# Kernel optimization log

Hardware: AMD Instinct MI355X
Metric: run time of the kernel (lower is better)

The kernel has to match this reference:

```python
import jax, jax.numpy as jnp
import numpy as np

FEATURE_DIM = 64
VALUE_DIM = 64
BATCH_HEADS = 64
SEQ_LEN = 4096


def setup_inputs() -> dict:
    key = jax.random.key(0)
    kq, kk, kv = jax.random.split(key, 3)
    q = jax.random.normal(kq, (BATCH_HEADS, SEQ_LEN, FEATURE_DIM), dtype=jnp.float32)
    k = jax.random.normal(kk, (BATCH_HEADS, SEQ_LEN, FEATURE_DIM), dtype=jnp.float32)
    v = jax.random.normal(kv, (BATCH_HEADS, SEQ_LEN, VALUE_DIM), dtype=jnp.float32)
    return {"q": q, "k": k, "v": v}


def reference(q, k, v):
    # q,k: (BH, S, F); v: (BH, S, V)
    # Recurrence: w_t = w_{t-1} + k_t v_t^T ; out_t = (q_t . w_t) / (t+1)
    bh, seq_len, f = q.shape
    val = v.shape[-1]

    def step(w, qkv_t):
        q_t, k_t, v_t = qkv_t  # (BH,F), (BH,F), (BH,V)
        w = w + jnp.einsum('bf,bv->bfv', k_t, v_t)
        out_t = jnp.einsum('bf,bfv->bv', q_t, w)
        return w, out_t

    w0 = jnp.zeros((bh, f, val), dtype=q.dtype)
    # scan over the sequence axis (time-major)
    xs = (jnp.swapaxes(q, 0, 1), jnp.swapaxes(k, 0, 1), jnp.swapaxes(v, 0, 1))
    _, outs = jax.lax.scan(step, w0, xs)  # outs: (S, BH, V)
    denom = jnp.arange(1, seq_len + 1, dtype=q.dtype)[:, None, None]
    outs = outs / denom
    return jnp.swapaxes(outs, 0, 1)  # (BH, S, V)
```

## Files before the change

kernel.cpp:

```cpp
#include <hip/hip_runtime.h>


#define BH    64
#define SEQ   4096
#define FD    64
#define VD    64
#define CHUNK 64
#define NCH   (SEQ / CHUNK)

typedef __attribute__((ext_vector_type(8))) short  short8;
typedef __attribute__((ext_vector_type(4))) float  f32x4;

static __device__ __forceinline__ unsigned short f2bf(float f) {
    unsigned int u = __builtin_bit_cast(unsigned int, f);
    u += 0x7FFF + ((u >> 16) & 1);
    return (unsigned short)(u >> 16);
}
static __device__ __forceinline__ float bf2f(unsigned short h) {
    unsigned int u = ((unsigned int)h) << 16;
    return __builtin_bit_cast(float, u);
}

__global__ __launch_bounds__(256) void ttr_pass1(const float* __restrict__ k,
                                                 const float* __restrict__ v,
                                                 unsigned short* __restrict__ ST) {
    const int b  = blockIdx.x >> 6;
    const int ci = blockIdx.x & 63;
    __shared__ unsigned short KT[64][72];
    __shared__ unsigned short VT[64][72];
    const int tid = threadIdx.x;
    const float* kc = k + ((size_t)b * SEQ + (size_t)ci * CHUNK) * FD;
    const float* vc = v + ((size_t)b * SEQ + (size_t)ci * CHUNK) * FD;

    #pragma unroll
    for (int i = tid; i < 64 * 16; i += 256) {
        const int s = i >> 4, f4 = (i & 15) << 2;
        float4 kv = *(const float4*)(kc + s * FD + f4);
        float4 vv = *(const float4*)(vc + s * FD + f4);
        KT[f4 + 0][s] = f2bf(kv.x); KT[f4 + 1][s] = f2bf(kv.y);
        KT[f4 + 2][s] = f2bf(kv.z); KT[f4 + 3][s] = f2bf(kv.w);
        VT[f4 + 0][s] = f2bf(vv.x); VT[f4 + 1][s] = f2bf(vv.y);
        VT[f4 + 2][s] = f2bf(vv.z); VT[f4 + 3][s] = f2bf(vv.w);
    }
    __syncthreads();

    const int wid  = tid >> 6;
    const int lane = tid & 63;
    const int mrow = lane & 15;
    const int kb   = (lane >> 4) << 3;

    f32x4 acc[4] = {};
    #pragma unroll
    for (int ks = 0; ks < 2; ks++) {
        short8 a = *(const short8*)&VT[16 * wid + mrow][ks * 32 + kb];
        #pragma unroll
        for (int cf = 0; cf < 4; cf++) {
            short8 bb = *(const short8*)&KT[16 * cf + mrow][ks * 32 + kb];
            acc[cf] = __builtin_amdgcn_mfma_f32_16x16x32_bf16(a, bb, acc[cf], 0, 0, 0);
        }
    }
    unsigned short* outp = ST + (size_t)(b * NCH + ci) * (VD * FD);
    const int vrow0 = 16 * wid + ((lane >> 4) << 2);
    const int fcol  = lane & 15;
    #pragma unroll
    for (int cf = 0; cf < 4; cf++)
        #pragma unroll
        for (int r = 0; r < 4; r++)
            outp[(size_t)(vrow0 + r) * FD + cf * 16 + fcol] = f2bf(acc[cf][r]);
}

__global__ __launch_bounds__(256) void ttr_pass2(unsigned short* __restrict__ ST) {
    const int b = blockIdx.x >> 4;
    const int e = ((blockIdx.x & 15) << 8) + threadIdx.x;
    unsigned short* p = ST + (size_t)b * NCH * (VD * FD) + e;
    float acc = 0.f;
    #pragma unroll 8
    for (int ci = 0; ci < NCH; ci++) {
        unsigned short s = p[(size_t)ci * (VD * FD)];
        p[(size_t)ci * (VD * FD)] = f2bf(acc);
        acc += bf2f(s);
    }
}

__global__ __launch_bounds__(256) void ttr_pass3(const float* __restrict__ q,
                                                 const float* __restrict__ k,
                                                 const float* __restrict__ v,
                                                 const unsigned short* __restrict__ WT,
                                                 float* __restrict__ out) {
    const int b  = blockIdx.x >> 6;
    const int ci = blockIdx.x & 63;
    __shared__ unsigned short Qs[64][72];
    __shared__ unsigned short Ks[64][72];
    __shared__ unsigned short VTs[64][136];
    __shared__ unsigned short Ps[4][16][72];
    const int tid = threadIdx.x;
    const float* qc = q + ((size_t)b * SEQ + (size_t)ci * CHUNK) * FD;
    const float* kc = k + ((size_t)b * SEQ + (size_t)ci * CHUNK) * FD;
    const float* vc = v + ((size_t)b * SEQ + (size_t)ci * CHUNK) * FD;

    #pragma unroll
    for (int i = tid; i < 64 * 16; i += 256) {
        const int t = i >> 4, f4 = (i & 15) << 2;
        float4 qv = *(const float4*)(qc + t * FD + f4);
        float4 kv = *(const float4*)(kc + t * FD + f4);
        float4 vv = *(const float4*)(vc + t * FD + f4);
        Qs[t][f4 + 0] = f2bf(qv.x); Qs[t][f4 + 1] = f2bf(qv.y);
        Qs[t][f4 + 2] = f2bf(qv.z); Qs[t][f4 + 3] = f2bf(qv.w);
        Ks[t][f4 + 0] = f2bf(kv.x); Ks[t][f4 + 1] = f2bf(kv.y);
        Ks[t][f4 + 2] = f2bf(kv.z); Ks[t][f4 + 3] = f2bf(kv.w);
        VTs[f4 + 0][t] = f2bf(vv.x); VTs[f4 + 1][t] = f2bf(vv.y);
        VTs[f4 + 2][t] = f2bf(vv.z); VTs[f4 + 3][t] = f2bf(vv.w);
    }
    const unsigned short* wsrc = WT + (size_t)(b * NCH + ci) * (VD * FD);
    #pragma unroll
    for (int i = tid; i < 512; i += 256) {
        const int vv = i >> 3, f8 = (i & 7) << 3;
        *(uint4*)&VTs[vv][64 + f8] = *(const uint4*)(wsrc + vv * FD + f8);
    }
    __syncthreads();

    const int wid  = tid >> 6;
    const int lane = tid & 63;
    const int mrow = lane & 15;
    const int kb   = (lane >> 4) << 3;

    f32x4 pacc[4] = {};
    #pragma unroll
    for (int ks = 0; ks < 2; ks++) {
        short8 a = *(const short8*)&Qs[16 * wid + mrow][ks * 32 + kb];
        #pragma unroll
        for (int cf = 0; cf < 4; cf++) {
            short8 bb = *(const short8*)&Ks[16 * cf + mrow][ks * 32 + kb];
            pacc[cf] = __builtin_amdgcn_mfma_f32_16x16x32_bf16(a, bb, pacc[cf], 0, 0, 0);
        }
    }
    const int prow0 = (lane >> 4) << 2;
    const int pcol  = lane & 15;
    #pragma unroll
    for (int cf = 0; cf < 4; cf++)
        #pragma unroll
        for (int r = 0; r < 4; r++) {
            const int row_local = 16 * wid + prow0 + r;
            const int col       = cf * 16 + pcol;
            const float val = (col <= row_local) ? pacc[cf][r] : 0.f;
            Ps[wid][prow0 + r][cf * 16 + pcol] = f2bf(val);
        }
    __syncthreads();

    f32x4 oacc[4] = {};
    #pragma unroll
    for (int ks = 0; ks < 4; ks++) {
        short8 a;
        if (ks < 2) a = *(const short8*)&Ps[wid][mrow][ks * 32 + kb];
        else        a = *(const short8*)&Qs[16 * wid + mrow][(ks - 2) * 32 + kb];
        #pragma unroll
        for (int cn = 0; cn < 4; cn++) {
            short8 bb = *(const short8*)&VTs[16 * cn + mrow][ks * 32 + kb];
            oacc[cn] = __builtin_amdgcn_mfma_f32_16x16x32_bf16(a, bb, oacc[cn], 0, 0, 0);
        }
    }
    float* oc = out + ((size_t)b * SEQ + (size_t)ci * CHUNK) * VD;
    #pragma unroll
    for (int cn = 0; cn < 4; cn++)
        #pragma unroll
        for (int r = 0; r < 4; r++) {
            const int row_local = 16 * wid + prow0 + r;
            const float den = (float)(ci * CHUNK + row_local + 1);
            oc[(size_t)row_local * VD + cn * 16 + pcol] = oacc[cn][r] / den;
        }
}

extern "C" void kernel_launch(void* const* d_in, const int* in_sizes, int n_in,
                              void* d_out, int out_size, void* d_ws, size_t ws_size,
                              hipStream_t stream) {
    const float* q = (const float*)d_in[0];
    const float* k = (const float*)d_in[1];
    const float* v = (const float*)d_in[2];
    float* out = (float*)d_out;
    unsigned short* ST = (unsigned short*)d_ws;

    ttr_pass1<<<BH * NCH, 256, 0, stream>>>(k, v, ST);
    ttr_pass2<<<BH * (SEQ / CHUNK / 4), 256, 0, stream>>>(ST);
    ttr_pass3<<<BH * NCH, 256, 0, stream>>>(q, k, v, ST, out);
}
```

Measured before the change: 258.4 us.

## Merge prefix-scan into main pass, double chunk size to 128

Removes the separate prefix-sum kernel: each main-pass block now sums all earlier chunk states itself before running the intra-chunk attention. The chunk size goes from 64 to 128, so there are half as many states and the intra-chunk causal matmul doubles. Blocks grow to 512 threads, use packed bf16 conversion, stage chunk sums through shared memory for coalesced stores, and remap block indices so heads interleave. The price is redundant state-summing work, which grows with chunk index and is quadratic in the number of chunks, plus higher shared memory use per block.

```diff
diff --git a/kernel.cpp b/kernel.cpp
--- a/kernel.cpp
+++ b/kernel.cpp
@@ -1,12 +1,12 @@
 #include <hip/hip_runtime.h>
 
 
-#define BH    64
-#define SEQ   4096
-#define FD    64
-#define VD    64
-#define CHUNK 64
-#define NCH   (SEQ / CHUNK)
+#define BH   64
+#define SEQ  4096
+#define FD   64
+#define VD   64
+#define C    128
+#define NCH  (SEQ / C)
 
 typedef __attribute__((ext_vector_type(8))) short  short8;
 typedef __attribute__((ext_vector_type(4))) float  f32x4;
@@ -20,27 +20,39 @@
     unsigned int u = ((unsigned int)h) << 16;
     return __builtin_bit_cast(float, u);
 }
-
-__global__ __launch_bounds__(256) void ttr_pass1(const float* __restrict__ k,
-                                                 const float* __restrict__ v,
-                                                 unsigned short* __restrict__ ST) {
-    const int b  = blockIdx.x >> 6;
-    const int ci = blockIdx.x & 63;
-    __shared__ unsigned short KT[64][72];
-    __shared__ unsigned short VT[64][72];
+static __device__ __forceinline__ unsigned int pk2(float lo, float hi) {
+    unsigned int a = __builtin_bit_cast(unsigned int, lo);
+    unsigned int b = __builtin_bit_cast(unsigned int, hi);
+    a += 0x7FFF + ((a >> 16) & 1);
+    b += 0x7FFF + ((b >> 16) & 1);
+    return (a >> 16) | (b & 0xFFFF0000u);
+}
+
+__global__ __launch_bounds__(512, 4) void ttr_sums(const float* __restrict__ k,
+                                                   const float* __restrict__ v,
+                                                   unsigned short* __restrict__ ST) {
+    const int b  = blockIdx.x >> 5;
+    const int ci = blockIdx.x & 31;
+    __shared__ unsigned short KT[64][136];
+    __shared__ unsigned short VT[64][136];
+    __shared__ unsigned short Cs[64][72];
     const int tid = threadIdx.x;
-    const float* kc = k + ((size_t)b * SEQ + (size_t)ci * CHUNK) * FD;
-    const float* vc = v + ((size_t)b * SEQ + (size_t)ci * CHUNK) * FD;
-
-    #pragma unroll
-    for (int i = tid; i < 64 * 16; i += 256) {
-        const int s = i >> 4, f4 = (i & 15) << 2;
-        float4 kv = *(const float4*)(kc + s * FD + f4);
-        float4 vv = *(const float4*)(vc + s * FD + f4);
-        KT[f4 + 0][s] = f2bf(kv.x); KT[f4 + 1][s] = f2bf(kv.y);
-        KT[f4 + 2][s] = f2bf(kv.z); KT[f4 + 3][s] = f2bf(kv.w);
-        VT[f4 + 0][s] = f2bf(vv.x); VT[f4 + 1][s] = f2bf(vv.y);
-        VT[f4 + 2][s] = f2bf(vv.z); VT[f4 + 3][s] = f2bf(vv.w);
+    const float* kc = k + ((size_t)b * SEQ + (size_t)ci * C) * FD;
+    const float* vc = v + ((size_t)b * SEQ + (size_t)ci * C) * FD;
+
+    #pragma unroll
+    for (int it = 0; it < 4; ++it) {
+        const int i = tid + it * 512;
+        const int f = i & 63, t4 = (i >> 6) << 2;
+        float k0 = kc[(t4+0)*FD + f], k1 = kc[(t4+1)*FD + f];
+        float k2 = kc[(t4+2)*FD + f], k3 = kc[(t4+3)*FD + f];
+        float v0 = vc[(t4+0)*FD + f], v1 = vc[(t4+1)*FD + f];
+        float v2 = vc[(t4+2)*FD + f], v3 = vc[(t4+3)*FD + f];
+        uint2 kw, vw;
+        kw.x = pk2(k0, k1); kw.y = pk2(k2, k3);
+        vw.x = pk2(v0, v1); vw.y = pk2(v2, v3);
+        *(uint2*)&KT[f][t4] = kw;
+        *(uint2*)&VT[f][t4] = vw;
     }
     __syncthreads();
 
@@ -49,73 +61,90 @@
     const int mrow = lane & 15;
     const int kb   = (lane >> 4) << 3;
 
-    f32x4 acc[4] = {};
-    #pragma unroll
-    for (int ks = 0; ks < 2; ks++) {
-        short8 a = *(const short8*)&VT[16 * wid + mrow][ks * 32 + kb];
-        #pragma unroll
-        for (int cf = 0; cf < 4; cf++) {
-            short8 bb = *(const short8*)&KT[16 * cf + mrow][ks * 32 + kb];
-            acc[cf] = __builtin_amdgcn_mfma_f32_16x16x32_bf16(a, bb, acc[cf], 0, 0, 0);
-        }
-    }
+    if (wid < 4) {
+        f32x4 acc[4] = {};
+        #pragma unroll
+        for (int ks = 0; ks < 4; ++ks) {
+            short8 a = *(const short8*)&VT[16 * wid + mrow][ks * 32 + kb];
+            #pragma unroll
+            for (int cf = 0; cf < 4; ++cf) {
+                short8 bb = *(const short8*)&KT[16 * cf + mrow][ks * 32 + kb];
+                acc[cf] = __builtin_amdgcn_mfma_f32_16x16x32_bf16(a, bb, acc[cf], 0, 0, 0);
+            }
+        }
+        const int vrow0 = 16 * wid + ((lane >> 4) << 2);
+        const int fcol  = lane & 15;
+        #pragma unroll
+        for (int cf = 0; cf < 4; ++cf)
+            #pragma unroll
+            for (int r = 0; r < 4; ++r)
+                Cs[vrow0 + r][cf * 16 + fcol] = f2bf(acc[cf][r]);
+    }
+    __syncthreads();
+
     unsigned short* outp = ST + (size_t)(b * NCH + ci) * (VD * FD);
-    const int vrow0 = 16 * wid + ((lane >> 4) << 2);
-    const int fcol  = lane & 15;
-    #pragma unroll
-    for (int cf = 0; cf < 4; cf++)
-        #pragma unroll
-        for (int r = 0; r < 4; r++)
-            outp[(size_t)(vrow0 + r) * FD + cf * 16 + fcol] = f2bf(acc[cf][r]);
-}
-
-__global__ __launch_bounds__(256) void ttr_pass2(unsigned short* __restrict__ ST) {
-    const int b = blockIdx.x >> 4;
-    const int e = ((blockIdx.x & 15) << 8) + threadIdx.x;
-    unsigned short* p = ST + (size_t)b * NCH * (VD * FD) + e;
-    float acc = 0.f;
-    #pragma unroll 8
-    for (int ci = 0; ci < NCH; ci++) {
-        unsigned short s = p[(size_t)ci * (VD * FD)];
-        p[(size_t)ci * (VD * FD)] = f2bf(acc);
-        acc += bf2f(s);
-    }
-}
-
-__global__ __launch_bounds__(256) void ttr_pass3(const float* __restrict__ q,
-                                                 const float* __restrict__ k,
-                                                 const float* __restrict__ v,
-                                                 const unsigned short* __restrict__ WT,
-                                                 float* __restrict__ out) {
-    const int b  = blockIdx.x >> 6;
-    const int ci = blockIdx.x & 63;
-    __shared__ unsigned short Qs[64][72];
-    __shared__ unsigned short Ks[64][72];
-    __shared__ unsigned short VTs[64][136];
-    __shared__ unsigned short Ps[4][16][72];
+    const int rr = tid >> 3, c8 = (tid & 7) << 3;
+    *(uint4*)(outp + rr * FD + c8) = *(const uint4*)&Cs[rr][c8];
+}
+
+__global__ __launch_bounds__(512, 4) void ttr_main(const float* __restrict__ q,
+                                                   const float* __restrict__ k,
+                                                   const float* __restrict__ v,
+                                                   const unsigned short* __restrict__ ST,
+                                                   float* __restrict__ out) {
+    const unsigned bid = blockIdx.x;
+    const int b  = (int)(((bid & 7u) << 3) | (bid >> 8));
+    const int ci = (int)((bid >> 3) & 31u);
+
+    __shared__ unsigned short POOL[8 * 16 * 136];
+    __shared__ unsigned short Qs[128][72];
+    __shared__ unsigned short VTs[64][200];
     const int tid = threadIdx.x;
-    const float* qc = q + ((size_t)b * SEQ + (size_t)ci * CHUNK) * FD;
-    const float* kc = k + ((size_t)b * SEQ + (size_t)ci * CHUNK) * FD;
-    const float* vc = v + ((size_t)b * SEQ + (size_t)ci * CHUNK) * FD;
-
-    #pragma unroll
-    for (int i = tid; i < 64 * 16; i += 256) {
-        const int t = i >> 4, f4 = (i & 15) << 2;
-        float4 qv = *(const float4*)(qc + t * FD + f4);
-        float4 kv = *(const float4*)(kc + t * FD + f4);
-        float4 vv = *(const float4*)(vc + t * FD + f4);
-        Qs[t][f4 + 0] = f2bf(qv.x); Qs[t][f4 + 1] = f2bf(qv.y);
-        Qs[t][f4 + 2] = f2bf(qv.z); Qs[t][f4 + 3] = f2bf(qv.w);
-        Ks[t][f4 + 0] = f2bf(kv.x); Ks[t][f4 + 1] = f2bf(kv.y);
-        Ks[t][f4 + 2] = f2bf(kv.z); Ks[t][f4 + 3] = f2bf(kv.w);
-        VTs[f4 + 0][t] = f2bf(vv.x); VTs[f4 + 1][t] = f2bf(vv.y);
-        VTs[f4 + 2][t] = f2bf(vv.z); VTs[f4 + 3][t] = f2bf(vv.w);
-    }
-    const unsigned short* wsrc = WT + (size_t)(b * NCH + ci) * (VD * FD);
-    #pragma unroll
-    for (int i = tid; i < 512; i += 256) {
-        const int vv = i >> 3, f8 = (i & 7) << 3;
-        *(uint4*)&VTs[vv][64 + f8] = *(const uint4*)(wsrc + vv * FD + f8);
+    const float* qc = q + ((size_t)b * SEQ + (size_t)ci * C) * FD;
+    const float* kc = k + ((size_t)b * SEQ + (size_t)ci * C) * FD;
+    const float* vc = v + ((size_t)b * SEQ + (size_t)ci * C) * FD;
+
+    {
+        float wa[8] = {0.f, 0.f, 0.f, 0.f, 0.f, 0.f, 0.f, 0.f};
+        const unsigned short* stb = ST + (size_t)b * NCH * (VD * FD) + tid * 8;
+        for (int cj = 0; cj < ci; ++cj) {
+            short8 s = *(const short8*)(stb + (size_t)cj * (VD * FD));
+            #pragma unroll
+            for (int j = 0; j < 8; ++j) wa[j] += bf2f((unsigned short)s[j]);
+        }
+        const int vv = tid >> 3, f0 = (tid & 7) << 3;
+        uint4 wv;
+        wv.x = pk2(wa[0], wa[1]); wv.y = pk2(wa[2], wa[3]);
+        wv.z = pk2(wa[4], wa[5]); wv.w = pk2(wa[6], wa[7]);
+        *(uint4*)&VTs[vv][128 + f0] = wv;
+    }
+
+    #pragma unroll
+    for (int it = 0; it < 2; ++it) {
+        const int i = tid + it * 512;
+        const int t = i >> 3, f8 = (i & 7) << 3;
+        float4 q0 = *(const float4*)(qc + t * FD + f8);
+        float4 q1 = *(const float4*)(qc + t * FD + f8 + 4);
+        float4 k0 = *(const float4*)(kc + t * FD + f8);
+        float4 k1 = *(const float4*)(kc + t * FD + f8 + 4);
+        uint4 qw, kw;
+        qw.x = pk2(q0.x, q0.y); qw.y = pk2(q0.z, q0.w);
+        qw.z = pk2(q1.x, q1.y); qw.w = pk2(q1.z, q1.w);
+        kw.x = pk2(k0.x, k0.y); kw.y = pk2(k0.z, k0.w);
+        kw.z = pk2(k1.x, k1.y); kw.w = pk2(k1.z, k1.w);
+        *(uint4*)&Qs[t][f8] = qw;
+        *(uint4*)&POOL[t * 72 + f8] = kw;
+    }
+
+    #pragma unroll
+    for (int it = 0; it < 4; ++it) {
+        const int i = tid + it * 512;
+        const int f = i & 63, t4 = (i >> 6) << 2;
+        float v0 = vc[(t4+0)*FD + f], v1 = vc[(t4+1)*FD + f];
+        float v2 = vc[(t4+2)*FD + f], v3 = vc[(t4+3)*FD + f];
+        uint2 vw;
+        vw.x = pk2(v0, v1); vw.y = pk2(v2, v3);
+        *(uint2*)&VTs[f][t4] = vw;
     }
     __syncthreads();
 
@@ -124,48 +153,51 @@
     const int mrow = lane & 15;
     const int kb   = (lane >> 4) << 3;
 
-    f32x4 pacc[4] = {};
-    #pragma unroll
-    for (int ks = 0; ks < 2; ks++) {
+    f32x4 pacc[8] = {};
+    #pragma unroll
+    for (int ks = 0; ks < 2; ++ks) {
         short8 a = *(const short8*)&Qs[16 * wid + mrow][ks * 32 + kb];
         #pragma unroll
-        for (int cf = 0; cf < 4; cf++) {
-            short8 bb = *(const short8*)&Ks[16 * cf + mrow][ks * 32 + kb];
+        for (int cf = 0; cf < 8; ++cf) {
+            short8 bb = *(const short8*)&POOL[(16 * cf + mrow) * 72 + ks * 32 + kb];
             pacc[cf] = __builtin_amdgcn_mfma_f32_16x16x32_bf16(a, bb, pacc[cf], 0, 0, 0);
         }
     }
+    __syncthreads();
+
     const int prow0 = (lane >> 4) << 2;
     const int pcol  = lane & 15;
     #pragma unroll
-    for (int cf = 0; cf < 4; cf++)
-        #pragma unroll
-        for (int r = 0; r < 4; r++) {
+    for (int cf = 0; cf < 8; ++cf)
+        #pragma unroll
+        for (int r = 0; r < 4; ++r) {
             const int row_local = 16 * wid + prow0 + r;
-            const int col       = cf * 16 + pcol;
+            const int col       = 16 * cf + pcol;
             const float val = (col <= row_local) ? pacc[cf][r] : 0.f;
-            Ps[wid][prow0 + r][cf * 16 + pcol] = f2bf(val);
+            POOL[(16 * wid + prow0 + r) * 136 + col] = f2bf(val);
         }
     __syncthreads();
 
     f32x4 oacc[4] = {};
     #pragma unroll
-    for (int ks = 0; ks < 4; ks++) {
+    for (int ks = 0; ks < 6; ++ks) {
         short8 a;
-        if (ks < 2) a = *(const short8*)&Ps[wid][mrow][ks * 32 + kb];
-        else        a = *(const short8*)&Qs[16 * wid + mrow][(ks - 2) * 32 + kb];
-        #pragma unroll
-        for (int cn = 0; cn < 4; cn++) {
+        if (ks < 4) a = *(const short8*)&POOL[(16 * wid + mrow) * 136 + ks * 32 + kb];
+        else        a = *(const short8*)&Qs[16 * wid + mrow][(ks - 4) * 32 + kb];
+        #pragma unroll
+        for (int cn = 0; cn < 4; ++cn) {
             short8 bb = *(const short8*)&VTs[16 * cn + mrow][ks * 32 + kb];
             oacc[cn] = __builtin_amdgcn_mfma_f32_16x16x32_bf16(a, bb, oacc[cn], 0, 0, 0);
         }
     }
-    float* oc = out + ((size_t)b * SEQ + (size_t)ci * CHUNK) * VD;
-    #pragma unroll
-    for (int cn = 0; cn < 4; cn++)
-        #pragma unroll
-        for (int r = 0; r < 4; r++) {
+
+    float* oc = out + ((size_t)b * SEQ + (size_t)ci * C) * VD;
+    #pragma unroll
+    for (int cn = 0; cn < 4; ++cn)
+        #pragma unroll
+        for (int r = 0; r < 4; ++r) {
             const int row_local = 16 * wid + prow0 + r;
-            const float den = (float)(ci * CHUNK + row_local + 1);
+            const float den = (float)(ci * C + row_local + 1);
             oc[(size_t)row_local * VD + cn * 16 + pcol] = oacc[cn][r] / den;
         }
 }
@@ -179,7 +211,6 @@
     float* out = (float*)d_out;
     unsigned short* ST = (unsigned short*)d_ws;
 
-    ttr_pass1<<<BH * NCH, 256, 0, stream>>>(k, v, ST);
-    ttr_pass2<<<BH * (SEQ / CHUNK / 4), 256, 0, stream>>>(ST);
-    ttr_pass3<<<BH * NCH, 256, 0, stream>>>(q, k, v, ST, out);
-}
+    ttr_sums<<<BH * NCH, 512, 0, stream>>>(k, v, ST);
+    ttr_main<<<BH * NCH, 512, 0, stream>>>(q, k, v, ST, out);
+}
```

Result: no change. 262.1 us (+1.4%).
